# Kernel optimization log

Measured on AMD Instinct MI355X. Metric: run time of the kernel, lower is better.

## Reference

```python
import jax, jax.numpy as jnp
import numpy as np

EPS = 1e-7  # keras backend epsilon

def setup_inputs() -> dict:
    key = jax.random.key(0)
    k1, k2, k3 = jax.random.split(key, 3)
    B, L, D, P = 16, 1024, 256, 20
    sent1 = jax.random.normal(k1, (B, L, D), dtype=jnp.float32)
    sent2 = jax.random.normal(k2, (B, L, D), dtype=jnp.float32)
    kernel = jax.random.normal(k3, (P, D), dtype=jnp.float32) * 0.1
    return {"sent1": sent1, "sent2": sent2, "kernel": kernel}

def reference(sent1, sent2, kernel):
    # token norms with keras-style clamping: sqrt(max(sum(x^2), eps))
    n1 = jnp.sqrt(jnp.maximum(jnp.sum(sent1 * sent1, axis=-1), EPS))  # [B,L1]
    n2 = jnp.sqrt(jnp.maximum(jnp.sum(sent2 * sent2, axis=-1), EPS))  # [B,L2]
    # all-pairs cosine matrix via matmul instead of broadcast-multiply-reduce
    dots = jnp.einsum('bld,bmd->blm', sent1, sent2)                    # [B,L1,L2]
    cos = dots / n1[:, :, None] / n2[:, None, :]
    # mean attentive vectors: cosine-weighted sum of sent2, normalized by row sum
    weighted = jnp.einsum('blm,bmd->bld', cos, sent2)                  # [B,L1,D]
    mav = weighted / (jnp.sum(cos, axis=-1, keepdims=True) + EPS)      # [B,L1,D]
    # perspective-weighted cosine between sent1*k and mav*k, fused without [B,L,P,D]
    k2 = kernel * kernel                                               # [P,D]
    num = jnp.einsum('bld,pd->blp', sent1 * mav, k2)                   # sum_d s1*mav*k^2
    nv1 = jnp.sqrt(jnp.maximum(jnp.einsum('bld,pd->blp', sent1 * sent1, k2), EPS))
    nv2 = jnp.sqrt(jnp.maximum(jnp.einsum('bld,pd->blp', mav * mav, k2), EPS))
    return num / nv1 / nv2                                             # [B,L1,P]
```

## Files before the change

### kernel.cpp

```cpp
#include <hip/hip_runtime.h>
#include <math.h>

#define EPS 1e-7f

constexpr int B = 16, L = 1024, D = 256, P = 20;
constexpr int LD = L * D;
constexpr int DD = D * D;

typedef __attribute__((ext_vector_type(8))) _Float16 f16x8;
typedef __attribute__((ext_vector_type(4))) float f32x4;


__device__ inline unsigned short f2h(float x) {
    _Float16 h = (_Float16)x;
    union { _Float16 h; unsigned short u; } c; c.h = h; return c.u;
}
__device__ inline float h2f(unsigned short u) {
    union { unsigned short u; _Float16 h; } c; c.u = u; return (float)c.h;
}

__global__ __launch_bounds__(256) void k_prep2(const float* __restrict__ s2,
                                               float* __restrict__ tp,
                                               unsigned short* __restrict__ CT) {
    __shared__ float tile[32][257];
    __shared__ float wiv[32];
    __shared__ float wsq[32];
    int tid = threadIdx.x;
    int b   = blockIdx.x >> 5, mt = blockIdx.x & 31;
    int m0  = mt * 32;
    {
        int r = tid >> 3, c0 = (tid & 7) * 32;
        const float* gp = s2 + (size_t)b * LD + (size_t)(m0 + r) * D + c0;
        float4 v[8];
#pragma unroll
        for (int q = 0; q < 8; ++q) v[q] = ((const float4*)gp)[q];
#pragma unroll
        for (int q = 0; q < 8; ++q) *(float4*)&tile[r][c0 + q * 4] = v[q];
    }
    __syncthreads();
    {
        int r = tid >> 3, seg = tid & 7;
        float s = 0.f;
#pragma unroll
        for (int k = 0; k < 32; ++k) { float v = tile[r][seg * 32 + k]; s += v * v; }
#pragma unroll
        for (int o = 4; o; o >>= 1) s += __shfl_down(s, o, 8);
        if (seg == 0) {
            float iv = 1.0f / sqrtf(fmaxf(s, EPS));
            wiv[r] = iv;
            wsq[r] = sqrtf(iv);
        }
    }
    __syncthreads();
    {
        int dc = tid;
        float tpart = 0.f;
        union { unsigned short us[32]; uint4 q[4]; } ph;
#pragma unroll
        for (int m = 0; m < 32; ++m) {
            float v = tile[m][dc];
            tpart += v * wiv[m];
            ph.us[m] = f2h(v * wsq[m]);
        }
        tp[(size_t)(mt * B + b) * D + dc] = tpart;
        size_t o = (size_t)b * LD + (size_t)dc * L + m0;
        *(uint4*)(CT + o)      = ph.q[0]; *(uint4*)(CT + o + 8)  = ph.q[1];
        *(uint4*)(CT + o + 16) = ph.q[2]; *(uint4*)(CT + o + 24) = ph.q[3];
    }
}

__global__ __launch_bounds__(256) void k_u(const float* __restrict__ s1,
                                           const float* __restrict__ tp,
                                           float* __restrict__ invU,
                                           unsigned short* __restrict__ s1f) {
    __shared__ float ts[D];
    int tid = threadIdx.x;
    {
        int b0 = (blockIdx.x * 4) >> 10;
        float acc = 0.f;
#pragma unroll
        for (int mc = 0; mc < 32; ++mc)
            acc += tp[(size_t)(mc * B + b0) * D + tid];
        ts[tid] = acc;
    }
    __syncthreads();

    int w = tid >> 6, lane = tid & 63;
    int row = blockIdx.x * 4 + w;
    int dg = lane & 15;

    float4 sv[4];
    float up = 0.f, sq = 0.f;
#pragma unroll
    for (int j = 0; j < 4; ++j) {
        sv[j] = *(const float4*)(s1 + (size_t)row * D + dg * 4 + j * 64);
        float4 tv = *(const float4*)(ts + dg * 4 + j * 64);
        up += sv[j].x * tv.x + sv[j].y * tv.y + sv[j].z * tv.z + sv[j].w * tv.w;
        sq += sv[j].x * sv[j].x + sv[j].y * sv[j].y + sv[j].z * sv[j].z + sv[j].w * sv[j].w;
    }
#pragma unroll
    for (int o = 8; o; o >>= 1) {
        up += __shfl_down(up, o, 16);
        sq += __shfl_down(sq, o, 16);
    }
    if (lane == 0) {
        float n1v = sqrtf(fmaxf(sq, EPS));
        invU[row] = 1.0f / (up + EPS * n1v);
    }
#pragma unroll
    for (int j = 0; j < 4; ++j) {
        ushort4 h4;
        h4.x = f2h(sv[j].x); h4.y = f2h(sv[j].y);
        h4.z = f2h(sv[j].z); h4.w = f2h(sv[j].w);
        *(ushort4*)(s1f + (size_t)row * D + dg * 4 + j * 64) = h4;
    }
}

__global__ __launch_bounds__(256) void k_gram_mfma(const unsigned short* __restrict__ CT,
                                                   float* __restrict__ Gp) {
    __shared__ short As[128 * 72];
    __shared__ short Bs[64 * 72];
    int tid  = threadIdx.x;
    int b    = blockIdx.x >> 5;
    int rem  = blockIdx.x & 31;
    int ti   = rem >> 4;
    int tj   = (rem >> 2) & 3;
    int kc   = rem & 3;
    int wave = tid >> 6, lane = tid & 63;
    int wr   = (wave >> 1) * 64, wcc = (wave & 1) * 32;
    int lr   = lane & 15, lq = lane >> 4;
    int arow = tid >> 1, ahalf = (tid & 1) * 32;
    int brow = tid >> 2, bq = (tid & 3) * 16;

    f32x4 acc[4][2];
#pragma unroll
    for (int i = 0; i < 4; ++i)
#pragma unroll
        for (int j = 0; j < 2; ++j) acc[i][j] = (f32x4){0.f, 0.f, 0.f, 0.f};

#pragma unroll 1
    for (int kb = 0; kb < 4; ++kb) {
        int koff = kc * 256 + kb * 64;
        __syncthreads();
        {
            const unsigned short* ga = CT + (size_t)b * LD + (size_t)(ti * 128 + arow) * L + koff + ahalf;
            uint4 a0 = ((const uint4*)ga)[0], a1 = ((const uint4*)ga)[1];
            uint4 a2 = ((const uint4*)ga)[2], a3 = ((const uint4*)ga)[3];
            const unsigned short* gb = CT + (size_t)b * LD + (size_t)(tj * 64 + brow) * L + koff + bq;
            uint4 b0 = ((const uint4*)gb)[0], b1 = ((const uint4*)gb)[1];
            short* la = &As[arow * 72 + ahalf];
            ((uint4*)la)[0] = a0; ((uint4*)la)[1] = a1;
            ((uint4*)la)[2] = a2; ((uint4*)la)[3] = a3;
            short* lb = &Bs[brow * 72 + bq];
            ((uint4*)lb)[0] = b0; ((uint4*)lb)[1] = b1;
        }
        __syncthreads();
#pragma unroll
        for (int ks = 0; ks < 2; ++ks) {
            f16x8 af[4], bfr[2];
#pragma unroll
            for (int i = 0; i < 4; ++i)
                af[i] = *(const f16x8*)&As[(wr + i * 16 + lr) * 72 + ks * 32 + lq * 8];
#pragma unroll
            for (int j = 0; j < 2; ++j)
                bfr[j] = *(const f16x8*)&Bs[(wcc + j * 16 + lr) * 72 + ks * 32 + lq * 8];
#pragma unroll
            for (int i = 0; i < 4; ++i)
#pragma unroll
                for (int j = 0; j < 2; ++j)
                    acc[i][j] = __builtin_amdgcn_mfma_f32_16x16x32_f16(af[i], bfr[j], acc[i][j], 0, 0, 0);
        }
    }
    float* gout = Gp + ((size_t)(kc * B + b)) * DD;
#pragma unroll
    for (int i = 0; i < 4; ++i)
#pragma unroll
        for (int r = 0; r < 4; ++r) {
            int row = ti * 128 + wr + i * 16 + lq * 4 + r;
#pragma unroll
            for (int j = 0; j < 2; ++j)
                gout[(size_t)row * D + tj * 64 + wcc + j * 16 + lr] = acc[i][j][r];
        }
}

__global__ __launch_bounds__(256) void k_reduceG(const float* __restrict__ Gp,
                                                 unsigned short* __restrict__ Gf) {
    size_t i = ((size_t)blockIdx.x * 256 + threadIdx.x) * 4;
    float4 s = *(const float4*)(Gp + i);
#pragma unroll
    for (int kc = 1; kc < 4; ++kc) {
        float4 a = *(const float4*)(Gp + (size_t)kc * B * DD + i);
        s.x += a.x; s.y += a.y; s.z += a.z; s.w += a.w;
    }
    ushort4 h4;
    h4.x = f2h(s.x); h4.y = f2h(s.y); h4.z = f2h(s.z); h4.w = f2h(s.w);
    *(ushort4*)(Gf + i) = h4;
}

__global__ __launch_bounds__(256) void k_mav_mfma(const unsigned short* __restrict__ s1f,
                                                  const unsigned short* __restrict__ Gf,
                                                  unsigned short* __restrict__ mavh) {
    __shared__ short As[64 * 72];
    __shared__ short Bs[128 * 72];
    int tid  = threadIdx.x;
    int b    = blockIdx.x >> 5;
    int rem  = blockIdx.x & 31;
    int lt   = rem >> 1, nt = rem & 1;
    int l0   = lt * 64, n0 = nt * 128;
    int wave = tid >> 6, lane = tid & 63;
    int wn   = wave * 32;
    int lr   = lane & 15, lq = lane >> 4;
    int arow = tid >> 2, aq = (tid & 3) * 16;
    int brow = tid >> 1, bhalf = (tid & 1) * 32;

    f32x4 acc[4][2];
#pragma unroll
    for (int i = 0; i < 4; ++i)
#pragma unroll
        for (int j = 0; j < 2; ++j) acc[i][j] = (f32x4){0.f, 0.f, 0.f, 0.f};

#pragma unroll 1
    for (int kb = 0; kb < 4; ++kb) {
        int koff = kb * 64;
        __syncthreads();
        {
            const unsigned short* ga = s1f + (size_t)(b * L + l0 + arow) * D + koff + aq;
            uint4 a0 = ((const uint4*)ga)[0], a1 = ((const uint4*)ga)[1];
            const unsigned short* gb = Gf + (size_t)b * DD + (size_t)(n0 + brow) * D + koff + bhalf;
            uint4 b0 = ((const uint4*)gb)[0], b1 = ((const uint4*)gb)[1];
            uint4 b2 = ((const uint4*)gb)[2], b3 = ((const uint4*)gb)[3];
            short* la = &As[arow * 72 + aq];
            ((uint4*)la)[0] = a0; ((uint4*)la)[1] = a1;
            short* lb = &Bs[brow * 72 + bhalf];
            ((uint4*)lb)[0] = b0; ((uint4*)lb)[1] = b1;
            ((uint4*)lb)[2] = b2; ((uint4*)lb)[3] = b3;
        }
        __syncthreads();
#pragma unroll
        for (int ks = 0; ks < 2; ++ks) {
            f16x8 af[4], bfr[2];
#pragma unroll
            for (int i = 0; i < 4; ++i)
                af[i] = *(const f16x8*)&As[(i * 16 + lr) * 72 + ks * 32 + lq * 8];
#pragma unroll
            for (int j = 0; j < 2; ++j)
                bfr[j] = *(const f16x8*)&Bs[(wn + j * 16 + lr) * 72 + ks * 32 + lq * 8];
#pragma unroll
            for (int i = 0; i < 4; ++i)
#pragma unroll
                for (int j = 0; j < 2; ++j)
                    acc[i][j] = __builtin_amdgcn_mfma_f32_16x16x32_f16(af[i], bfr[j], acc[i][j], 0, 0, 0);
        }
    }
#pragma unroll
    for (int i = 0; i < 4; ++i)
#pragma unroll
        for (int r = 0; r < 4; ++r) {
            int l = l0 + i * 16 + lq * 4 + r;
#pragma unroll
            for (int j = 0; j < 2; ++j)
                mavh[(size_t)(b * L + l) * D + n0 + wn + j * 16 + lr] = f2h(acc[i][j][r]);
        }
}

__global__ __launch_bounds__(256) void k_out(const unsigned short* __restrict__ s1f,
                                             const unsigned short* __restrict__ mavh,
                                             const float* __restrict__ invU,
                                             const float* __restrict__ kern,
                                             float* __restrict__ out) {
    __shared__ float k2s[P * D];
    int tid = threadIdx.x;
#pragma unroll
    for (int p = 0; p < P; ++p) {
        float v = kern[p * D + tid];
        k2s[p * D + tid] = v * v;
    }
    __syncthreads();

    int w = tid >> 6, lane = tid & 63;
    int row = blockIdx.x * 4 + w;
    int dg = lane & 15, ps = lane >> 4;

    float4 sm[4], ss[4], mm[4];
#pragma unroll
    for (int j = 0; j < 4; ++j) {
        ushort4 h4 = *(const ushort4*)(s1f + (size_t)row * D + dg * 4 + j * 64);
        ushort4 m4 = *(const ushort4*)(mavh + (size_t)row * D + dg * 4 + j * 64);
        float4 sv, mv;
        sv.x = h2f(h4.x); sv.y = h2f(h4.y); sv.z = h2f(h4.z); sv.w = h2f(h4.w);
        mv.x = h2f(m4.x); mv.y = h2f(m4.y); mv.z = h2f(m4.z); mv.w = h2f(m4.w);
        sm[j].x = sv.x * mv.x; sm[j].y = sv.y * mv.y; sm[j].z = sv.z * mv.z; sm[j].w = sv.w * mv.w;
        ss[j].x = sv.x * sv.x; ss[j].y = sv.y * sv.y; ss[j].z = sv.z * sv.z; ss[j].w = sv.w * sv.w;
        mm[j].x = mv.x * mv.x; mm[j].y = mv.y * mv.y; mm[j].z = mv.z * mv.z; mm[j].w = mv.w * mv.w;
    }
    float sgn = (invU[row] < 0.f) ? -1.f : 1.f;
#pragma unroll
    for (int tI = 0; tI < 5; ++tI) {
        int p = ps + tI * 4;
        float na = 0.f, nb = 0.f, nc = 0.f;
#pragma unroll
        for (int j = 0; j < 4; ++j) {
            float4 kv = *(const float4*)&k2s[p * D + j * 64 + dg * 4];
            na += sm[j].x * kv.x + sm[j].y * kv.y + sm[j].z * kv.z + sm[j].w * kv.w;
            nb += ss[j].x * kv.x + ss[j].y * kv.y + ss[j].z * kv.z + ss[j].w * kv.w;
            nc += mm[j].x * kv.x + mm[j].y * kv.y + mm[j].z * kv.z + mm[j].w * kv.w;
        }
#pragma unroll
        for (int o = 8; o; o >>= 1) {
            na += __shfl_down(na, o, 16);
            nb += __shfl_down(nb, o, 16);
            nc += __shfl_down(nc, o, 16);
        }
        if (dg == 0) {
            out[(size_t)row * P + p] = sgn * na * rsqrtf(fmaxf(nb, EPS)) *
                                       rsqrtf(fmaxf(nc, EPS));
        }
    }
}

extern "C" void kernel_launch(void* const* d_in, const int* in_sizes, int n_in,
                              void* d_out, int out_size, void* d_ws, size_t ws_size,
                              hipStream_t stream) {
    const float* s1   = (const float*)d_in[0];
    const float* s2   = (const float*)d_in[1];
    const float* kern = (const float*)d_in[2];
    float* out = (float*)d_out;
    float* ws  = (float*)d_ws;

    float* tp   = ws;
    float* invU = ws + 131072;
    unsigned short* s1f  = (unsigned short*)(ws + 147456);
    unsigned short* CT   = (unsigned short*)(ws + 2244608);
    unsigned short* Gf   = (unsigned short*)(ws + 4341760);
    float* Gp   = ws + 4866048;
    unsigned short* mavh = (unsigned short*)(ws + 9060352);

    k_prep2<<<512, 256, 0, stream>>>(s2, tp, CT);
    k_u<<<4096, 256, 0, stream>>>(s1, tp, invU, s1f);
    k_gram_mfma<<<512, 256, 0, stream>>>(CT, Gp);
    k_reduceG<<<1024, 256, 0, stream>>>(Gp, Gf);
    k_mav_mfma<<<512, 256, 0, stream>>>(s1f, Gf, mavh);
    k_out<<<4096, 256, 0, stream>>>(s1f, mavh, invU, kern, out);
}
```

Measured before the change: 128.7 us.

## Fuse mav MFMA GEMM with perspective-cosine output kernel via shared memory

Merges the mav GEMM and the output kernel into one kernel. Each block now computes a 32-row by full-256-column mav tile, stages it in LDS through a union with the GEMM buffers, and then computes the perspective cosines directly. This removes the fp16 mav round-trip through global memory and one kernel launch. In exchange the fused kernel launches fewer blocks (512), loads the whole G slice per block, recomputes k^2 for every block, and runs a serial 8-row epilogue per wave.

```diff
diff --git a/kernel.cpp b/kernel.cpp
--- a/kernel.cpp
+++ b/kernel.cpp
@@ -197,27 +197,31 @@
     *(ushort4*)(Gf + i) = h4;
 }
 
-__global__ __launch_bounds__(256) void k_mav_mfma(const unsigned short* __restrict__ s1f,
-                                                  const unsigned short* __restrict__ Gf,
-                                                  unsigned short* __restrict__ mavh) {
-    __shared__ short As[64 * 72];
-    __shared__ short Bs[128 * 72];
+union MoSh {
+    struct { short As[32 * 72]; short Bs[256 * 72]; } g;
+    struct { unsigned short mavs[32][264]; float k2s[P * D]; } e;
+};
+__global__ __launch_bounds__(256, 2) void k_mavout(const unsigned short* __restrict__ s1f,
+                                                   const unsigned short* __restrict__ Gf,
+                                                   const float* __restrict__ invU,
+                                                   const float* __restrict__ kern,
+                                                   float* __restrict__ out) {
+    __shared__ MoSh sh;
     int tid  = threadIdx.x;
     int b    = blockIdx.x >> 5;
-    int rem  = blockIdx.x & 31;
-    int lt   = rem >> 1, nt = rem & 1;
-    int l0   = lt * 64, n0 = nt * 128;
+    int lt   = blockIdx.x & 31;
+    int l0   = lt * 32;
     int wave = tid >> 6, lane = tid & 63;
-    int wn   = wave * 32;
+    int wn   = wave * 64;
     int lr   = lane & 15, lq = lane >> 4;
-    int arow = tid >> 2, aq = (tid & 3) * 16;
+    int arow = tid >> 3, aq = (tid & 7) * 8;
     int brow = tid >> 1, bhalf = (tid & 1) * 32;
 
-    f32x4 acc[4][2];
-#pragma unroll
-    for (int i = 0; i < 4; ++i)
-#pragma unroll
-        for (int j = 0; j < 2; ++j) acc[i][j] = (f32x4){0.f, 0.f, 0.f, 0.f};
+    f32x4 acc[2][4];
+#pragma unroll
+    for (int i = 0; i < 2; ++i)
+#pragma unroll
+        for (int j = 0; j < 4; ++j) acc[i][j] = (f32x4){0.f, 0.f, 0.f, 0.f};
 
 #pragma unroll 1
     for (int kb = 0; kb < 4; ++kb) {
@@ -225,95 +229,95 @@
         __syncthreads();
         {
             const unsigned short* ga = s1f + (size_t)(b * L + l0 + arow) * D + koff + aq;
-            uint4 a0 = ((const uint4*)ga)[0], a1 = ((const uint4*)ga)[1];
-            const unsigned short* gb = Gf + (size_t)b * DD + (size_t)(n0 + brow) * D + koff + bhalf;
-            uint4 b0 = ((const uint4*)gb)[0], b1 = ((const uint4*)gb)[1];
-            uint4 b2 = ((const uint4*)gb)[2], b3 = ((const uint4*)gb)[3];
-            short* la = &As[arow * 72 + aq];
-            ((uint4*)la)[0] = a0; ((uint4*)la)[1] = a1;
-            short* lb = &Bs[brow * 72 + bhalf];
-            ((uint4*)lb)[0] = b0; ((uint4*)lb)[1] = b1;
-            ((uint4*)lb)[2] = b2; ((uint4*)lb)[3] = b3;
+            uint4 a0 = *(const uint4*)ga;
+            *(uint4*)&sh.g.As[arow * 72 + aq] = a0;
+            const unsigned short* gb0 = Gf + (size_t)b * DD + (size_t)brow * D + koff + bhalf;
+            const unsigned short* gb1 = gb0 + (size_t)128 * D;
+            uint4 q0 = ((const uint4*)gb0)[0], q1 = ((const uint4*)gb0)[1];
+            uint4 q2 = ((const uint4*)gb0)[2], q3 = ((const uint4*)gb0)[3];
+            uint4 r0 = ((const uint4*)gb1)[0], r1 = ((const uint4*)gb1)[1];
+            uint4 r2 = ((const uint4*)gb1)[2], r3 = ((const uint4*)gb1)[3];
+            short* lb0 = &sh.g.Bs[brow * 72 + bhalf];
+            short* lb1 = &sh.g.Bs[(brow + 128) * 72 + bhalf];
+            ((uint4*)lb0)[0] = q0; ((uint4*)lb0)[1] = q1;
+            ((uint4*)lb0)[2] = q2; ((uint4*)lb0)[3] = q3;
+            ((uint4*)lb1)[0] = r0; ((uint4*)lb1)[1] = r1;
+            ((uint4*)lb1)[2] = r2; ((uint4*)lb1)[3] = r3;
         }
         __syncthreads();
 #pragma unroll
         for (int ks = 0; ks < 2; ++ks) {
-            f16x8 af[4], bfr[2];
-#pragma unroll
-            for (int i = 0; i < 4; ++i)
-                af[i] = *(const f16x8*)&As[(i * 16 + lr) * 72 + ks * 32 + lq * 8];
-#pragma unroll
-            for (int j = 0; j < 2; ++j)
-                bfr[j] = *(const f16x8*)&Bs[(wn + j * 16 + lr) * 72 + ks * 32 + lq * 8];
-#pragma unroll
-            for (int i = 0; i < 4; ++i)
-#pragma unroll
-                for (int j = 0; j < 2; ++j)
+            f16x8 af[2], bfr[4];
+#pragma unroll
+            for (int i = 0; i < 2; ++i)
+                af[i] = *(const f16x8*)&sh.g.As[(i * 16 + lr) * 72 + ks * 32 + lq * 8];
+#pragma unroll
+            for (int j = 0; j < 4; ++j)
+                bfr[j] = *(const f16x8*)&sh.g.Bs[(wn + j * 16 + lr) * 72 + ks * 32 + lq * 8];
+#pragma unroll
+            for (int i = 0; i < 2; ++i)
+#pragma unroll
+                for (int j = 0; j < 4; ++j)
                     acc[i][j] = __builtin_amdgcn_mfma_f32_16x16x32_f16(af[i], bfr[j], acc[i][j], 0, 0, 0);
         }
     }
-#pragma unroll
-    for (int i = 0; i < 4; ++i)
+
+    __syncthreads();
+#pragma unroll
+    for (int i = 0; i < 2; ++i)
 #pragma unroll
         for (int r = 0; r < 4; ++r) {
-            int l = l0 + i * 16 + lq * 4 + r;
-#pragma unroll
-            for (int j = 0; j < 2; ++j)
-                mavh[(size_t)(b * L + l) * D + n0 + wn + j * 16 + lr] = f2h(acc[i][j][r]);
-        }
-}
-
-__global__ __launch_bounds__(256) void k_out(const unsigned short* __restrict__ s1f,
-                                             const unsigned short* __restrict__ mavh,
-                                             const float* __restrict__ invU,
-                                             const float* __restrict__ kern,
-                                             float* __restrict__ out) {
-    __shared__ float k2s[P * D];
-    int tid = threadIdx.x;
+            int row = i * 16 + lq * 4 + r;
+#pragma unroll
+            for (int j = 0; j < 4; ++j)
+                sh.e.mavs[row][wn + j * 16 + lr] = f2h(acc[i][j][r]);
+        }
 #pragma unroll
     for (int p = 0; p < P; ++p) {
         float v = kern[p * D + tid];
-        k2s[p * D + tid] = v * v;
-    }
-    __syncthreads();
-
-    int w = tid >> 6, lane = tid & 63;
-    int row = blockIdx.x * 4 + w;
+        sh.e.k2s[p * D + tid] = v * v;
+    }
+    __syncthreads();
+
     int dg = lane & 15, ps = lane >> 4;
-
-    float4 sm[4], ss[4], mm[4];
-#pragma unroll
-    for (int j = 0; j < 4; ++j) {
-        ushort4 h4 = *(const ushort4*)(s1f + (size_t)row * D + dg * 4 + j * 64);
-        ushort4 m4 = *(const ushort4*)(mavh + (size_t)row * D + dg * 4 + j * 64);
-        float4 sv, mv;
-        sv.x = h2f(h4.x); sv.y = h2f(h4.y); sv.z = h2f(h4.z); sv.w = h2f(h4.w);
-        mv.x = h2f(m4.x); mv.y = h2f(m4.y); mv.z = h2f(m4.z); mv.w = h2f(m4.w);
-        sm[j].x = sv.x * mv.x; sm[j].y = sv.y * mv.y; sm[j].z = sv.z * mv.z; sm[j].w = sv.w * mv.w;
-        ss[j].x = sv.x * sv.x; ss[j].y = sv.y * sv.y; ss[j].z = sv.z * sv.z; ss[j].w = sv.w * sv.w;
-        mm[j].x = mv.x * mv.x; mm[j].y = mv.y * mv.y; mm[j].z = mv.z * mv.z; mm[j].w = mv.w * mv.w;
-    }
-    float sgn = (invU[row] < 0.f) ? -1.f : 1.f;
-#pragma unroll
-    for (int tI = 0; tI < 5; ++tI) {
-        int p = ps + tI * 4;
-        float na = 0.f, nb = 0.f, nc = 0.f;
+#pragma unroll 1
+    for (int rr = 0; rr < 8; ++rr) {
+        int mrow = wave * 8 + rr;
+        int gl   = b * L + l0 + mrow;
+        float4 sm[4], ss[4], mm[4];
 #pragma unroll
         for (int j = 0; j < 4; ++j) {
-            float4 kv = *(const float4*)&k2s[p * D + j * 64 + dg * 4];
-            na += sm[j].x * kv.x + sm[j].y * kv.y + sm[j].z * kv.z + sm[j].w * kv.w;
-            nb += ss[j].x * kv.x + ss[j].y * kv.y + ss[j].z * kv.z + ss[j].w * kv.w;
-            nc += mm[j].x * kv.x + mm[j].y * kv.y + mm[j].z * kv.z + mm[j].w * kv.w;
-        }
-#pragma unroll
-        for (int o = 8; o; o >>= 1) {
-            na += __shfl_down(na, o, 16);
-            nb += __shfl_down(nb, o, 16);
-            nc += __shfl_down(nc, o, 16);
-        }
-        if (dg == 0) {
-            out[(size_t)row * P + p] = sgn * na * rsqrtf(fmaxf(nb, EPS)) *
-                                       rsqrtf(fmaxf(nc, EPS));
+            ushort4 h4 = *(const ushort4*)(s1f + (size_t)gl * D + dg * 4 + j * 64);
+            ushort4 m4 = *(const ushort4*)&sh.e.mavs[mrow][dg * 4 + j * 64];
+            float4 sv, mv;
+            sv.x = h2f(h4.x); sv.y = h2f(h4.y); sv.z = h2f(h4.z); sv.w = h2f(h4.w);
+            mv.x = h2f(m4.x); mv.y = h2f(m4.y); mv.z = h2f(m4.z); mv.w = h2f(m4.w);
+            sm[j].x = sv.x * mv.x; sm[j].y = sv.y * mv.y; sm[j].z = sv.z * mv.z; sm[j].w = sv.w * mv.w;
+            ss[j].x = sv.x * sv.x; ss[j].y = sv.y * sv.y; ss[j].z = sv.z * sv.z; ss[j].w = sv.w * sv.w;
+            mm[j].x = mv.x * mv.x; mm[j].y = mv.y * mv.y; mm[j].z = mv.z * mv.z; mm[j].w = mv.w * mv.w;
+        }
+        float sgn = (invU[gl] < 0.f) ? -1.f : 1.f;
+#pragma unroll
+        for (int tI = 0; tI < 5; ++tI) {
+            int p = ps + tI * 4;
+            float na = 0.f, nb = 0.f, nc = 0.f;
+#pragma unroll
+            for (int j = 0; j < 4; ++j) {
+                float4 kv = *(const float4*)&sh.e.k2s[p * D + j * 64 + dg * 4];
+                na += sm[j].x * kv.x + sm[j].y * kv.y + sm[j].z * kv.z + sm[j].w * kv.w;
+                nb += ss[j].x * kv.x + ss[j].y * kv.y + ss[j].z * kv.z + ss[j].w * kv.w;
+                nc += mm[j].x * kv.x + mm[j].y * kv.y + mm[j].z * kv.z + mm[j].w * kv.w;
+            }
+#pragma unroll
+            for (int o = 8; o; o >>= 1) {
+                na += __shfl_down(na, o, 16);
+                nb += __shfl_down(nb, o, 16);
+                nc += __shfl_down(nc, o, 16);
+            }
+            if (dg == 0) {
+                out[(size_t)gl * P + p] = sgn * na * rsqrtf(fmaxf(nb, EPS)) *
+                                          rsqrtf(fmaxf(nc, EPS));
+            }
         }
     }
 }
@@ -329,16 +333,14 @@
 
     float* tp   = ws;
     float* invU = ws + 131072;
-    unsigned short* s1f  = (unsigned short*)(ws + 147456);
-    unsigned short* CT   = (unsigned short*)(ws + 2244608);
-    unsigned short* Gf   = (unsigned short*)(ws + 4341760);
+    unsigned short* s1f = (unsigned short*)(ws + 147456);
+    unsigned short* CT  = (unsigned short*)(ws + 2244608);
+    unsigned short* Gf  = (unsigned short*)(ws + 4341760);
     float* Gp   = ws + 4866048;
-    unsigned short* mavh = (unsigned short*)(ws + 9060352);
 
     k_prep2<<<512, 256, 0, stream>>>(s2, tp, CT);
     k_u<<<4096, 256, 0, stream>>>(s1, tp, invU, s1f);
     k_gram_mfma<<<512, 256, 0, stream>>>(CT, Gp);
     k_reduceG<<<1024, 256, 0, stream>>>(Gp, Gf);
-    k_mav_mfma<<<512, 256, 0, stream>>>(s1f, Gf, mavh);
-    k_out<<<4096, 256, 0, stream>>>(s1f, mavh, invU, kern, out);
-}
+    k_mavout<<<512, 256, 0, stream>>>(s1f, Gf, invU, kern, out);
+}
```

Result: slower. 133.2 us (+3.5%).
